# Kernel tuning notes

Hardware: AMD Instinct MI355X
Metric: run time of the kernel (lower is better)

## Reference

```python
import jax, jax.numpy as jnp
import numpy as np

N, E, C_IN, C_HID, C_OUT = 50000, 800000, 128, 64, 40


def _glorot(key, fan_in, fan_out):
    lim = np.sqrt(6.0 / (fan_in + fan_out)).astype(np.float32)
    return jax.random.uniform(key, (fan_in, fan_out), jnp.float32, -lim, lim)


def setup_inputs() -> dict:
    key = jax.random.key(0)
    kf, ks, ko, k1, k2 = jax.random.split(key, 5)
    features = jax.random.normal(kf, (N, C_IN), jnp.float32)
    src = jax.random.randint(ks, (E,), 0, N, jnp.int64 if jax.config.jax_enable_x64 else jnp.int32)
    # guarantee no self loops so add_remaining_self_loops == append full diagonal
    off = jax.random.randint(ko, (E,), 0, N - 1, src.dtype)
    dst = (src + 1 + off) % N
    return {
        "features": features,
        "src": src,
        "dst": dst,
        "W1": _glorot(k1, C_IN, C_HID),
        "b1": jnp.zeros((C_HID,), jnp.float32),
        "W2": _glorot(k2, C_HID, C_OUT),
        "b2": jnp.zeros((C_OUT,), jnp.float32),
    }


def reference(features, src, dst, W1, b1, W2, b2):
    n = features.shape[0]
    loop = jnp.arange(n, dtype=src.dtype)
    s = jnp.concatenate([src, loop])  # source nodes j (with self loops)
    d = jnp.concatenate([dst, loop])  # target nodes i
    ones = jnp.ones(s.shape[0], features.dtype)
    deg = jax.ops.segment_sum(ones, d, num_segments=n)  # in-degree incl. loop, >=1
    dinv = jax.lax.rsqrt(deg)
    norm = dinv[s] * dinv[d]  # D^{-1/2} A_hat D^{-1/2}, per edge

    def gcn_conv(x, W, b):
        h = x @ W  # [n, out]
        msgs = norm[:, None] * h[s]  # edge-wise gather + scale
        return jax.ops.segment_sum(msgs, d, num_segments=n) + b  # scatter-add

    x = jax.nn.relu(gcn_conv(features, W1, b1))
    # dropout: eval mode (training=False) -> identity
    x = gcn_conv(x, W2, b2)
    return jax.nn.log_softmax(x, axis=1)
```

## Files before the change

### kernel.cpp

```cpp
#include <hip/hip_runtime.h>
#include <math.h>

#define C_IN  128
#define C_HID 64
#define C_OUT 40
#define H1DW  32
#define H2DW  20

#define BKT_SH 7
#define BKT_N  (1 << BKT_SH)
#define CHUNK  1024
#define EPT    (CHUNK / 256)

__device__ __forceinline__ float bf2f(unsigned short u) {
    return __uint_as_float(((unsigned int)u) << 16);
}
__device__ __forceinline__ unsigned short f2bf(float f) {
    unsigned int x = __float_as_uint(f);
    return (unsigned short)((x + 0x7FFFu + ((x >> 16) & 1u)) >> 16);
}

__global__ void k_hist(const int* __restrict__ dst, int* __restrict__ hist2d, int e, int nbkt) {
    __shared__ int hist[512];
    for (int i = threadIdx.x; i < nbkt; i += 256) hist[i] = 0;
    __syncthreads();
    int base = blockIdx.x * CHUNK;
#pragma unroll
    for (int j = 0; j < EPT; ++j) {
        int i = base + j * 256 + threadIdx.x;
        if (i < e) atomicAdd(&hist[dst[i] >> BKT_SH], 1);
    }
    __syncthreads();
    int* row = hist2d + (size_t)blockIdx.x * nbkt;
    for (int i = threadIdx.x; i < nbkt; i += 256) row[i] = hist[i];
}

__global__ void k_bktscan(const int* __restrict__ hist2d, int* __restrict__ base2d,
                          int* __restrict__ tot, int nchunks, int nbkt) {
    __shared__ int wtot[4];
    const int b = blockIdx.x;
    const int t = threadIdx.x;
    const int lane = t & 63, wv = t >> 6;
    int carry = 0;
    for (int c0 = 0; c0 < nchunks; c0 += 256) {
        int c = c0 + t;
        int v = (c < nchunks) ? hist2d[(size_t)c * nbkt + b] : 0;
        int inc = v;
        for (int o = 1; o < 64; o <<= 1) { int u = __shfl_up(inc, o); if (lane >= o) inc += u; }
        if (lane == 63) wtot[wv] = inc;
        __syncthreads();
        int add = carry;
        for (int k = 0; k < wv; ++k) add += wtot[k];
        if (c < nchunks) base2d[(size_t)c * nbkt + b] = add + inc - v;
        carry += wtot[0] + wtot[1] + wtot[2] + wtot[3];
        __syncthreads();
    }
    if (t == 0) tot[b] = carry;
}

__global__ void k_scan_bkt(const int* __restrict__ tot, int* __restrict__ bstart, int nbkt, int e) {
    __shared__ int wtot[4];
    const int t = threadIdx.x;
    const int lane = t & 63, wv = t >> 6;
    int carry = 0;
    for (int b0 = 0; b0 < nbkt; b0 += 256) {
        int b = b0 + t;
        int v = (b < nbkt) ? tot[b] : 0;
        int inc = v;
        for (int o = 1; o < 64; o <<= 1) { int u = __shfl_up(inc, o); if (lane >= o) inc += u; }
        if (lane == 63) wtot[wv] = inc;
        __syncthreads();
        int add = carry;
        for (int k = 0; k < wv; ++k) add += wtot[k];
        if (b < nbkt) bstart[b] = add + inc - v;
        carry += wtot[0] + wtot[1] + wtot[2] + wtot[3];
        __syncthreads();
    }
    if (t == 0) bstart[nbkt] = e;
}

__global__ void k_binA(const int* __restrict__ src, const int* __restrict__ dst,
                       const int* __restrict__ bstart, const int* __restrict__ hist2d,
                       const int* __restrict__ base2d, unsigned int* __restrict__ bpack,
                       int e, int nbkt) {
    __shared__ int hist[512];
    __shared__ int excl[512];
    __shared__ int gbase[512];
    __shared__ int wtot[4];
    __shared__ unsigned int stage[CHUNK];
    const int t = threadIdx.x;
    const int base = blockIdx.x * CHUNK;
    const int lane = t & 63, wv = t >> 6;

    int carry = 0;
    for (int b0 = 0; b0 < nbkt; b0 += 256) {
        int b = b0 + t;
        int v = (b < nbkt) ? hist2d[(size_t)blockIdx.x * nbkt + b] : 0;
        int inc = v;
        for (int o = 1; o < 64; o <<= 1) { int u = __shfl_up(inc, o); if (lane >= o) inc += u; }
        if (lane == 63) wtot[wv] = inc;
        __syncthreads();
        int add = carry;
        for (int k = 0; k < wv; ++k) add += wtot[k];
        if (b < nbkt) {
            excl[b]  = add + inc - v;
            hist[b]  = 0;
            gbase[b] = bstart[b] + base2d[(size_t)blockIdx.x * nbkt + b];
        }
        carry += wtot[0] + wtot[1] + wtot[2] + wtot[3];
        __syncthreads();
    }

#pragma unroll
    for (int j = 0; j < EPT; ++j) {
        int i = base + j * 256 + t;
        if (i < e) {
            int d = dst[i];
            unsigned int pk = (unsigned int)src[i] | ((unsigned int)d << 16);
            int bk = d >> BKT_SH;
            int p  = excl[bk] + atomicAdd(&hist[bk], 1);
            stage[p] = pk;
        }
    }
    __syncthreads();

    int nchunk = min(CHUNK, e - base);
    for (int i = t; i < nchunk; i += 256) {
        unsigned int u = stage[i];
        int b = (int)(u >> 16) >> BKT_SH;
        bpack[gbase[b] + (i - excl[b])] = u;
    }
}

__global__ void k_binB(const int* __restrict__ bstart, const unsigned int* __restrict__ bpack,
                       int* __restrict__ row_start, float* __restrict__ dinv,
                       int* __restrict__ csr_src, int n, int e, int nbkt) {
    __shared__ int hist[BKT_N];
    __shared__ int excl[BKT_N];
    __shared__ int wtot[4];
    const int t = threadIdx.x;
    const int b = blockIdx.x;
    const int beg = bstart[b], end = bstart[b + 1];
    const int nodebase = b << BKT_SH;
    const int nloc = min(BKT_N, n - nodebase);

    for (int i = t; i < nloc; i += 256) hist[i] = 0;
    __syncthreads();
    for (int i = beg + t; i < end; i += 256)
        atomicAdd(&hist[(int)(bpack[i] >> 16) - nodebase], 1);
    __syncthreads();

    {
        int idx = t;
        int v = (idx < nloc) ? hist[idx] : 0;
        int inc = v; int lane = t & 63; int wv = t >> 6;
        for (int o = 1; o < 64; o <<= 1) { int u = __shfl_up(inc, o); if (lane >= o) inc += u; }
        if (lane == 63) wtot[wv] = inc;
        __syncthreads();
        int add = 0;
        for (int k = 0; k < wv; ++k) add += wtot[k];
        if (idx < nloc) excl[idx] = add + inc - v;
    }
    __syncthreads();

    for (int i = t; i < nloc; i += 256) {
        row_start[nodebase + i] = beg + excl[i];
        dinv[nodebase + i] = rsqrtf((float)hist[i] + 1.0f);
    }
    if (b == nbkt - 1 && t == 0) row_start[n] = e;
    __syncthreads();
    for (int i = t; i < nloc; i += 256) hist[i] = 0;
    __syncthreads();

    for (int i = beg + t; i < end; i += 256) {
        unsigned int u = bpack[i];
        int dl = (int)(u >> 16) - nodebase;
        int p = beg + excl[dl] + atomicAdd(&hist[dl], 1);
        csr_src[p] = (int)(u & 0xFFFFu);
    }
}

__global__ void k_gemm1(const float* __restrict__ X, const float* __restrict__ W1,
                        const float* __restrict__ dinv, unsigned short* __restrict__ h1b, int n) {
    __shared__ float xt[C_IN][64];
    __shared__ float wl[C_IN * C_HID];
    const int t = threadIdx.x;
    const int row0 = blockIdx.x * 64;

    for (int i = t; i < C_IN * C_HID; i += 256) wl[i] = W1[i];
    {
        int r = t >> 2, q = t & 3;
        int grow = row0 + r;
        for (int j = 0; j < 8; ++j) {
            int k = q * 32 + j * 4;
            float4 v = make_float4(0.f, 0.f, 0.f, 0.f);
            if (grow < n) v = *(const float4*)(X + (size_t)grow * C_IN + k);
            xt[k + 0][r] = v.x; xt[k + 1][r] = v.y; xt[k + 2][r] = v.z; xt[k + 3][r] = v.w;
        }
    }
    __syncthreads();

    const int rg = t >> 4, cg = t & 15;
    const int r0 = rg * 4, c0 = cg * 4;
    float acc[4][4] = {};
#pragma unroll 4
    for (int k = 0; k < C_IN; ++k) {
        float4 a = *(const float4*)&xt[k][r0];
        float4 b = *(const float4*)&wl[k * C_HID + c0];
        acc[0][0] = fmaf(a.x, b.x, acc[0][0]); acc[0][1] = fmaf(a.x, b.y, acc[0][1]);
        acc[0][2] = fmaf(a.x, b.z, acc[0][2]); acc[0][3] = fmaf(a.x, b.w, acc[0][3]);
        acc[1][0] = fmaf(a.y, b.x, acc[1][0]); acc[1][1] = fmaf(a.y, b.y, acc[1][1]);
        acc[1][2] = fmaf(a.y, b.z, acc[1][2]); acc[1][3] = fmaf(a.y, b.w, acc[1][3]);
        acc[2][0] = fmaf(a.z, b.x, acc[2][0]); acc[2][1] = fmaf(a.z, b.y, acc[2][1]);
        acc[2][2] = fmaf(a.z, b.z, acc[2][2]); acc[2][3] = fmaf(a.z, b.w, acc[2][3]);
        acc[3][0] = fmaf(a.w, b.x, acc[3][0]); acc[3][1] = fmaf(a.w, b.y, acc[3][1]);
        acc[3][2] = fmaf(a.w, b.z, acc[3][2]); acc[3][3] = fmaf(a.w, b.w, acc[3][3]);
    }
#pragma unroll
    for (int i = 0; i < 4; ++i) {
        int row = row0 + r0 + i;
        if (row < n) {
            float di = dinv[row];
            ushort4 o;
            o.x = f2bf(di * acc[i][0]); o.y = f2bf(di * acc[i][1]);
            o.z = f2bf(di * acc[i][2]); o.w = f2bf(di * acc[i][3]);
            *(ushort4*)(h1b + (size_t)row * C_HID + c0) = o;
        }
    }
}

__global__ void k_agg1(const int* __restrict__ row_start, const int* __restrict__ csr_src,
                       const unsigned short* __restrict__ h1b, const float* __restrict__ dinv,
                       const float* __restrict__ b1, unsigned int* __restrict__ out1d, int n) {
    const int t = threadIdx.x;
    const int wid  = t >> 6;
    const int lane = t & 63;
    const int node = blockIdx.x * 4 + wid;
    if (node >= n) return;

    const int h  = lane >> 5;
    const int c2 = lane & 31;
    const unsigned int* h1d = (const unsigned int*)h1b;

    int beg = row_start[node], end = row_start[node + 1];
    float alo[4] = {0.f, 0.f, 0.f, 0.f}, ahi[4] = {0.f, 0.f, 0.f, 0.f};
    {
        unsigned int u = h1d[(size_t)node * H1DW + c2];
        if (h == 0) {
            alo[0] = __uint_as_float(u << 16);
            ahi[0] = __uint_as_float(u & 0xFFFF0000u);
        }
    }
    for (int j = beg; j < end; j += 64) {
        int sv = (j + lane < end) ? csr_src[j + lane] : 0;
        int m  = min(64, end - j);
        for (int k = 0; k < m; k += 8) {
#pragma unroll
            for (int i = 0; i < 4; ++i) {
                int idx = k + 2 * i + h;
                int s   = __shfl(sv, idx);
                float f = (idx < m) ? 1.f : 0.f;
                unsigned int u = h1d[(size_t)s * H1DW + c2];
                alo[i] = fmaf(f, __uint_as_float(u << 16), alo[i]);
                ahi[i] = fmaf(f, __uint_as_float(u & 0xFFFF0000u), ahi[i]);
            }
        }
    }
    float lo = (alo[0] + alo[1]) + (alo[2] + alo[3]);
    float hi = (ahi[0] + ahi[1]) + (ahi[2] + ahi[3]);
    lo += __shfl_xor(lo, 32);
    hi += __shfl_xor(hi, 32);

    if (h == 0) {
        float di = dinv[node];
        float2 bb = *(const float2*)(b1 + 2 * c2);
        float vlo = di * lo + bb.x;
        float vhi = di * hi + bb.y;
        vlo = vlo > 0.f ? vlo : 0.f;
        vhi = vhi > 0.f ? vhi : 0.f;
        out1d[(size_t)node * H1DW + c2] =
            (unsigned int)f2bf(vlo) | ((unsigned int)f2bf(vhi) << 16);
    }
}

__global__ void k_gemm2(const unsigned int* __restrict__ out1d, const float* __restrict__ W2,
                        const float* __restrict__ dinv, unsigned int* __restrict__ h2d, int n) {
    __shared__ float xt[C_HID][96];
    __shared__ float wl[C_HID * C_OUT];
    const int t = threadIdx.x;
    const int row0 = blockIdx.x * 96;

    for (int i = t; i < C_HID * C_OUT; i += 256) wl[i] = W2[i];
    for (int idx = t; idx < 96 * H1DW; idx += 256) {
        int r = idx >> 5, d = idx & 31;
        int grow = row0 + r;
        unsigned int u = (grow < n) ? out1d[(size_t)grow * H1DW + d] : 0u;
        xt[2 * d][r]     = __uint_as_float(u << 16);
        xt[2 * d + 1][r] = __uint_as_float(u & 0xFFFF0000u);
    }
    __syncthreads();

    if (t >= 240) return;
    const int rg = t / 10, cg = t - rg * 10;
    const int r0 = rg * 4, c0 = cg * 4;
    float acc[4][4] = {};
#pragma unroll 4
    for (int k = 0; k < C_HID; ++k) {
        float4 a = *(const float4*)&xt[k][r0];
        float4 b = *(const float4*)&wl[k * C_OUT + c0];
        acc[0][0] = fmaf(a.x, b.x, acc[0][0]); acc[0][1] = fmaf(a.x, b.y, acc[0][1]);
        acc[0][2] = fmaf(a.x, b.z, acc[0][2]); acc[0][3] = fmaf(a.x, b.w, acc[0][3]);
        acc[1][0] = fmaf(a.y, b.x, acc[1][0]); acc[1][1] = fmaf(a.y, b.y, acc[1][1]);
        acc[1][2] = fmaf(a.y, b.z, acc[1][2]); acc[1][3] = fmaf(a.y, b.w, acc[1][3]);
        acc[2][0] = fmaf(a.z, b.x, acc[2][0]); acc[2][1] = fmaf(a.z, b.y, acc[2][1]);
        acc[2][2] = fmaf(a.z, b.z, acc[2][2]); acc[2][3] = fmaf(a.z, b.w, acc[2][3]);
        acc[3][0] = fmaf(a.w, b.x, acc[3][0]); acc[3][1] = fmaf(a.w, b.y, acc[3][1]);
        acc[3][2] = fmaf(a.w, b.z, acc[3][2]); acc[3][3] = fmaf(a.w, b.w, acc[3][3]);
    }
#pragma unroll
    for (int i = 0; i < 4; ++i) {
        int row = row0 + r0 + i;
        if (row < n) {
            float di = dinv[row];
            unsigned int u0 = (unsigned int)f2bf(di * acc[i][0]) | ((unsigned int)f2bf(di * acc[i][1]) << 16);
            unsigned int u1 = (unsigned int)f2bf(di * acc[i][2]) | ((unsigned int)f2bf(di * acc[i][3]) << 16);
            h2d[(size_t)row * H2DW + (c0 >> 1)]     = u0;
            h2d[(size_t)row * H2DW + (c0 >> 1) + 1] = u1;
        }
    }
}

__global__ void k_agg2(const int* __restrict__ row_start, const int* __restrict__ csr_src,
                       const unsigned short* __restrict__ h2b, const float* __restrict__ dinv,
                       const float* __restrict__ b2, float* __restrict__ out, int n) {
    int node = (blockIdx.x * 256 + threadIdx.x) >> 6;
    int lane = threadIdx.x & 63;
    if (node >= n) return;
    const int h3 = lane / 20;
    const int c2 = lane - h3 * 20;
    const unsigned int* h2d = (const unsigned int*)h2b;

    int beg = row_start[node], end = row_start[node + 1];
    float alo[4] = {0.f, 0.f, 0.f, 0.f}, ahi[4] = {0.f, 0.f, 0.f, 0.f};
    if (h3 == 0) {
        unsigned int u = h2d[(size_t)node * H2DW + c2];
        alo[0] = __uint_as_float(u << 16);
        ahi[0] = __uint_as_float(u & 0xFFFF0000u);
    }
    for (int j = beg; j < end; j += 64) {
        int sv = (j + lane < end) ? csr_src[j + lane] : 0;
        int m = min(64, end - j);
        for (int k = 0; k < m; k += 12) {
#pragma unroll
            for (int i = 0; i < 4; ++i) {
                int idx = k + 3 * i + h3;
                int s = __shfl(sv, idx & 63);
                float f = (idx < m) ? 1.f : 0.f;
                unsigned int u = h2d[(size_t)s * H2DW + c2];
                alo[i] = fmaf(f, __uint_as_float(u << 16), alo[i]);
                ahi[i] = fmaf(f, __uint_as_float(u & 0xFFFF0000u), ahi[i]);
            }
        }
    }
    float lo = (alo[0] + alo[1]) + (alo[2] + alo[3]);
    float hi = (ahi[0] + ahi[1]) + (ahi[2] + ahi[3]);
    float lA = __shfl(lo, c2 + 20), lB = __shfl(lo, c2 + 40);
    float hA = __shfl(hi, c2 + 20), hB = __shfl(hi, c2 + 40);
    lo += lA + lB;
    hi += hA + hB;

    float di = dinv[node];
    float vlo = -INFINITY, vhi = -INFINITY, ex = 0.f;
    if (h3 == 0) {
        float2 bb = *(const float2*)(b2 + 2 * c2);
        vlo = di * lo + bb.x;
        vhi = di * hi + bb.y;
    }
    float mx = fmaxf(vlo, vhi);
    for (int off = 16; off; off >>= 1) mx = fmaxf(mx, __shfl_xor(mx, off));
    if (h3 == 0) ex = expf(vlo - mx) + expf(vhi - mx);
    float ss = ex;
    for (int off = 16; off; off >>= 1) ss += __shfl_xor(ss, off);
    float lse = mx + logf(ss);
    if (h3 == 0)
        *(float2*)(out + (size_t)node * C_OUT + 2 * c2) = make_float2(vlo - lse, vhi - lse);
}

extern "C" void kernel_launch(void* const* d_in, const int* in_sizes, int n_in,
                              void* d_out, int out_size, void* d_ws, size_t ws_size,
                              hipStream_t stream) {
    const float* X   = (const float*)d_in[0];
    const int*   src = (const int*)d_in[1];
    const int*   dst = (const int*)d_in[2];
    const float* W1  = (const float*)d_in[3];
    const float* b1  = (const float*)d_in[4];
    const float* W2  = (const float*)d_in[5];
    const float* b2  = (const float*)d_in[6];
    float* out = (float*)d_out;

    const int N = in_sizes[0] / C_IN;
    const int E = in_sizes[1];
    const int NBKT = (N + BKT_N - 1) >> BKT_SH;
    const int nchunks = (E + CHUNK - 1) / CHUNK;

    char* ws = (char*)d_ws;
    size_t off = 0;
    auto take = [&](size_t bytes) { char* p = ws + off; off = (off + bytes + 255) & ~(size_t)255; return p; };
    int*   hist2d    = (int*)  take((size_t)nchunks * NBKT * 4);
    int*   base2d    = (int*)  take((size_t)nchunks * NBKT * 4);
    int*   tot       = (int*)  take(512 * 4);
    int*   bstart    = (int*)  take(512 * 4);
    unsigned int* bpack = (unsigned int*)take((size_t)E * 4);
    int*   csr_src   = (int*)  take((size_t)E * 4);
    int*   row_start = (int*)  take((size_t)(N + 1) * 4);
    float* dinv      = (float*)take((size_t)N * 4);
    unsigned short* h1b  = (unsigned short*)take((size_t)N * C_HID * 2);
    unsigned int*   out1 = (unsigned int*)  take((size_t)N * H1DW * 4);
    unsigned int*   h2d  = (unsigned int*)  take((size_t)N * H2DW * 4);

    k_hist    <<<nchunks, 256, 0, stream>>>(dst, hist2d, E, NBKT);
    k_bktscan <<<NBKT, 256, 0, stream>>>(hist2d, base2d, tot, nchunks, NBKT);
    k_scan_bkt<<<1, 256, 0, stream>>>(tot, bstart, NBKT, E);
    k_binA    <<<nchunks, 256, 0, stream>>>(src, dst, bstart, hist2d, base2d, bpack, E, NBKT);
    k_binB    <<<NBKT, 256, 0, stream>>>(bstart, bpack, row_start, dinv, csr_src, N, E, NBKT);

    k_gemm1   <<<(N + 63) / 64, 256, 0, stream>>>(X, W1, dinv, h1b, N);
    k_agg1    <<<(N + 3) / 4, 256, 0, stream>>>(row_start, csr_src, h1b, dinv, b1, out1, N);
    k_gemm2   <<<(N + 95) / 96, 256, 0, stream>>>(out1, W2, dinv, h2d, N);
    k_agg2    <<<((size_t)N * 64 + 255) / 256, 256, 0, stream>>>(row_start, csr_src,
                                                                 (const unsigned short*)h2d, dinv, b2, out, N);
}
```

Before: 123.9 us.

## Split feature tables into column halves and aggregate each half in separate passes

The bf16 feature tables for both layers are split into low and high column halves stored as separate arrays. Each aggregation runs as two passes, each gathering only half the columns. The intent is to shrink the randomly gathered working set so each half fits better in L2/MALL. The cost is reading the CSR twice, more kernel launches, and an extra float2 buffer passed between the two layer-2 passes before log_softmax.

```diff
diff --git a/kernel.cpp b/kernel.cpp
--- a/kernel.cpp
+++ b/kernel.cpp
@@ -4,17 +4,14 @@
 #define C_IN  128
 #define C_HID 64
 #define C_OUT 40
-#define H1DW  32
-#define H2DW  20
 
 #define BKT_SH 7
 #define BKT_N  (1 << BKT_SH)
 #define CHUNK  1024
 #define EPT    (CHUNK / 256)
 
-__device__ __forceinline__ float bf2f(unsigned short u) {
-    return __uint_as_float(((unsigned int)u) << 16);
-}
+__device__ __forceinline__ float bfLO(unsigned int u) { return __uint_as_float(u << 16); }
+__device__ __forceinline__ float bfHI(unsigned int u) { return __uint_as_float(u & 0xFFFF0000u); }
 __device__ __forceinline__ unsigned short f2bf(float f) {
     unsigned int x = __float_as_uint(f);
     return (unsigned short)((x + 0x7FFFu + ((x >> 16) & 1u)) >> 16);
@@ -181,7 +178,8 @@
 }
 
 __global__ void k_gemm1(const float* __restrict__ X, const float* __restrict__ W1,
-                        const float* __restrict__ dinv, unsigned short* __restrict__ h1b, int n) {
+                        const float* __restrict__ dinv,
+                        unsigned short* __restrict__ h1lo, unsigned short* __restrict__ h1hi, int n) {
     __shared__ float xt[C_IN][64];
     __shared__ float wl[C_IN * C_HID];
     const int t = threadIdx.x;
@@ -224,79 +222,72 @@
             ushort4 o;
             o.x = f2bf(di * acc[i][0]); o.y = f2bf(di * acc[i][1]);
             o.z = f2bf(di * acc[i][2]); o.w = f2bf(di * acc[i][3]);
-            *(ushort4*)(h1b + (size_t)row * C_HID + c0) = o;
-        }
-    }
-}
-
-__global__ void k_agg1(const int* __restrict__ row_start, const int* __restrict__ csr_src,
-                       const unsigned short* __restrict__ h1b, const float* __restrict__ dinv,
-                       const float* __restrict__ b1, unsigned int* __restrict__ out1d, int n) {
-    const int t = threadIdx.x;
-    const int wid  = t >> 6;
-    const int lane = t & 63;
+            if (c0 < 32) *(ushort4*)(h1lo + (size_t)row * 32 + c0)        = o;
+            else         *(ushort4*)(h1hi + (size_t)row * 32 + (c0 - 32)) = o;
+        }
+    }
+}
+
+template<int HALF>
+__global__ void k_agg1h(const int* __restrict__ row_start, const int* __restrict__ csr_src,
+                        const unsigned int* __restrict__ h1h, const float* __restrict__ dinv,
+                        const float* __restrict__ b1, unsigned int* __restrict__ out1h, int n) {
+    const int t = threadIdx.x;
+    const int wid = t >> 6, lane = t & 63;
     const int node = blockIdx.x * 4 + wid;
     if (node >= n) return;
-
-    const int h  = lane >> 5;
-    const int c2 = lane & 31;
-    const unsigned int* h1d = (const unsigned int*)h1b;
+    const int h4 = lane >> 4;
+    const int c2 = lane & 15;
 
     int beg = row_start[node], end = row_start[node + 1];
-    float alo[4] = {0.f, 0.f, 0.f, 0.f}, ahi[4] = {0.f, 0.f, 0.f, 0.f};
+    float alo0 = 0.f, ahi0 = 0.f, alo1 = 0.f, ahi1 = 0.f;
     {
-        unsigned int u = h1d[(size_t)node * H1DW + c2];
-        if (h == 0) {
-            alo[0] = __uint_as_float(u << 16);
-            ahi[0] = __uint_as_float(u & 0xFFFF0000u);
-        }
+        unsigned int u = h1h[(size_t)node * 16 + c2];
+        if (h4 == 0) { alo0 = bfLO(u); ahi0 = bfHI(u); }
     }
     for (int j = beg; j < end; j += 64) {
         int sv = (j + lane < end) ? csr_src[j + lane] : 0;
         int m  = min(64, end - j);
         for (int k = 0; k < m; k += 8) {
-#pragma unroll
-            for (int i = 0; i < 4; ++i) {
-                int idx = k + 2 * i + h;
-                int s   = __shfl(sv, idx);
-                float f = (idx < m) ? 1.f : 0.f;
-                unsigned int u = h1d[(size_t)s * H1DW + c2];
-                alo[i] = fmaf(f, __uint_as_float(u << 16), alo[i]);
-                ahi[i] = fmaf(f, __uint_as_float(u & 0xFFFF0000u), ahi[i]);
-            }
-        }
-    }
-    float lo = (alo[0] + alo[1]) + (alo[2] + alo[3]);
-    float hi = (ahi[0] + ahi[1]) + (ahi[2] + ahi[3]);
-    lo += __shfl_xor(lo, 32);
-    hi += __shfl_xor(hi, 32);
-
-    if (h == 0) {
+            int i0 = k + h4, i1 = k + 4 + h4;
+            int s0 = __shfl(sv, i0), s1 = __shfl(sv, i1);
+            float f0 = (i0 < m) ? 1.f : 0.f;
+            float f1 = (i1 < m) ? 1.f : 0.f;
+            unsigned int u0 = h1h[(size_t)s0 * 16 + c2];
+            unsigned int u1 = h1h[(size_t)s1 * 16 + c2];
+            alo0 = fmaf(f0, bfLO(u0), alo0); ahi0 = fmaf(f0, bfHI(u0), ahi0);
+            alo1 = fmaf(f1, bfLO(u1), alo1); ahi1 = fmaf(f1, bfHI(u1), ahi1);
+        }
+    }
+    float lo = alo0 + alo1, hi = ahi0 + ahi1;
+    lo += __shfl_xor(lo, 16); hi += __shfl_xor(hi, 16);
+    lo += __shfl_xor(lo, 32); hi += __shfl_xor(hi, 32);
+
+    if (h4 == 0) {
         float di = dinv[node];
-        float2 bb = *(const float2*)(b1 + 2 * c2);
-        float vlo = di * lo + bb.x;
-        float vhi = di * hi + bb.y;
-        vlo = vlo > 0.f ? vlo : 0.f;
-        vhi = vhi > 0.f ? vhi : 0.f;
-        out1d[(size_t)node * H1DW + c2] =
-            (unsigned int)f2bf(vlo) | ((unsigned int)f2bf(vhi) << 16);
-    }
-}
-
-__global__ void k_gemm2(const unsigned int* __restrict__ out1d, const float* __restrict__ W2,
-                        const float* __restrict__ dinv, unsigned int* __restrict__ h2d, int n) {
+        float2 bb = *(const float2*)(b1 + HALF * 32 + 2 * c2);
+        float vlo = fmaxf(fmaf(di, lo, bb.x), 0.f);
+        float vhi = fmaxf(fmaf(di, hi, bb.y), 0.f);
+        out1h[(size_t)node * 16 + c2] = (unsigned int)f2bf(vlo) | ((unsigned int)f2bf(vhi) << 16);
+    }
+}
+
+__global__ void k_gemm2(const unsigned int* __restrict__ o1lo, const unsigned int* __restrict__ o1hi,
+                        const float* __restrict__ W2, const float* __restrict__ dinv,
+                        unsigned int* __restrict__ h2lo, unsigned int* __restrict__ h2hi, int n) {
     __shared__ float xt[C_HID][96];
     __shared__ float wl[C_HID * C_OUT];
     const int t = threadIdx.x;
     const int row0 = blockIdx.x * 96;
 
     for (int i = t; i < C_HID * C_OUT; i += 256) wl[i] = W2[i];
-    for (int idx = t; idx < 96 * H1DW; idx += 256) {
-        int r = idx >> 5, d = idx & 31;
+    for (int idx = t; idx < 96 * 16; idx += 256) {
+        int r = idx >> 4, d = idx & 15;
         int grow = row0 + r;
-        unsigned int u = (grow < n) ? out1d[(size_t)grow * H1DW + d] : 0u;
-        xt[2 * d][r]     = __uint_as_float(u << 16);
-        xt[2 * d + 1][r] = __uint_as_float(u & 0xFFFF0000u);
+        unsigned int ulo = (grow < n) ? o1lo[(size_t)grow * 16 + d] : 0u;
+        unsigned int uhi = (grow < n) ? o1hi[(size_t)grow * 16 + d] : 0u;
+        xt[2 * d][r]      = bfLO(ulo); xt[2 * d + 1][r]  = bfHI(ulo);
+        xt[32 + 2 * d][r] = bfLO(uhi); xt[33 + 2 * d][r] = bfHI(uhi);
     }
     __syncthreads();
 
@@ -324,66 +315,84 @@
             float di = dinv[row];
             unsigned int u0 = (unsigned int)f2bf(di * acc[i][0]) | ((unsigned int)f2bf(di * acc[i][1]) << 16);
             unsigned int u1 = (unsigned int)f2bf(di * acc[i][2]) | ((unsigned int)f2bf(di * acc[i][3]) << 16);
-            h2d[(size_t)row * H2DW + (c0 >> 1)]     = u0;
-            h2d[(size_t)row * H2DW + (c0 >> 1) + 1] = u1;
-        }
-    }
-}
-
-__global__ void k_agg2(const int* __restrict__ row_start, const int* __restrict__ csr_src,
-                       const unsigned short* __restrict__ h2b, const float* __restrict__ dinv,
-                       const float* __restrict__ b2, float* __restrict__ out, int n) {
-    int node = (blockIdx.x * 256 + threadIdx.x) >> 6;
-    int lane = threadIdx.x & 63;
+            if (c0 < 20) {
+                h2lo[(size_t)row * 10 + (c0 >> 1)]     = u0;
+                h2lo[(size_t)row * 10 + (c0 >> 1) + 1] = u1;
+            } else {
+                h2hi[(size_t)row * 10 + ((c0 - 20) >> 1)]     = u0;
+                h2hi[(size_t)row * 10 + ((c0 - 20) >> 1) + 1] = u1;
+            }
+        }
+    }
+}
+
+template<int PASS>
+__global__ void k_agg2h(const int* __restrict__ row_start, const int* __restrict__ csr_src,
+                        const unsigned int* __restrict__ h2h, const float* __restrict__ dinv,
+                        const float* __restrict__ b2, float2* __restrict__ accLo,
+                        float* __restrict__ out, int n) {
+    const int t = threadIdx.x;
+    const int wid = t >> 6, lane = t & 63;
+    const int node = blockIdx.x * 4 + wid;
     if (node >= n) return;
-    const int h3 = lane / 20;
-    const int c2 = lane - h3 * 20;
-    const unsigned int* h2d = (const unsigned int*)h2b;
+    const int h6 = lane / 10;
+    const int c2 = lane - h6 * 10;
+    const bool act = h6 < 6;
 
     int beg = row_start[node], end = row_start[node + 1];
-    float alo[4] = {0.f, 0.f, 0.f, 0.f}, ahi[4] = {0.f, 0.f, 0.f, 0.f};
-    if (h3 == 0) {
-        unsigned int u = h2d[(size_t)node * H2DW + c2];
-        alo[0] = __uint_as_float(u << 16);
-        ahi[0] = __uint_as_float(u & 0xFFFF0000u);
+    float alo0 = 0.f, ahi0 = 0.f, alo1 = 0.f, ahi1 = 0.f;
+    if (h6 == 0) {
+        unsigned int u = h2h[(size_t)node * 10 + c2];
+        alo0 = bfLO(u); ahi0 = bfHI(u);
     }
     for (int j = beg; j < end; j += 64) {
         int sv = (j + lane < end) ? csr_src[j + lane] : 0;
-        int m = min(64, end - j);
+        int m  = min(64, end - j);
         for (int k = 0; k < m; k += 12) {
-#pragma unroll
-            for (int i = 0; i < 4; ++i) {
-                int idx = k + 3 * i + h3;
-                int s = __shfl(sv, idx & 63);
-                float f = (idx < m) ? 1.f : 0.f;
-                unsigned int u = h2d[(size_t)s * H2DW + c2];
-                alo[i] = fmaf(f, __uint_as_float(u << 16), alo[i]);
-                ahi[i] = fmaf(f, __uint_as_float(u & 0xFFFF0000u), ahi[i]);
-            }
-        }
-    }
-    float lo = (alo[0] + alo[1]) + (alo[2] + alo[3]);
-    float hi = (ahi[0] + ahi[1]) + (ahi[2] + ahi[3]);
-    float lA = __shfl(lo, c2 + 20), lB = __shfl(lo, c2 + 40);
-    float hA = __shfl(hi, c2 + 20), hB = __shfl(hi, c2 + 40);
-    lo += lA + lB;
-    hi += hA + hB;
-
-    float di = dinv[node];
-    float vlo = -INFINITY, vhi = -INFINITY, ex = 0.f;
-    if (h3 == 0) {
-        float2 bb = *(const float2*)(b2 + 2 * c2);
-        vlo = di * lo + bb.x;
-        vhi = di * hi + bb.y;
-    }
-    float mx = fmaxf(vlo, vhi);
-    for (int off = 16; off; off >>= 1) mx = fmaxf(mx, __shfl_xor(mx, off));
-    if (h3 == 0) ex = expf(vlo - mx) + expf(vhi - mx);
-    float ss = ex;
-    for (int off = 16; off; off >>= 1) ss += __shfl_xor(ss, off);
-    float lse = mx + logf(ss);
-    if (h3 == 0)
-        *(float2*)(out + (size_t)node * C_OUT + 2 * c2) = make_float2(vlo - lse, vhi - lse);
+            int i0 = k + h6, i1 = k + 6 + h6;
+            int s0 = __shfl(sv, i0 & 63), s1 = __shfl(sv, i1 & 63);
+            float f0 = (act && i0 < m) ? 1.f : 0.f;
+            float f1 = (act && i1 < m) ? 1.f : 0.f;
+            unsigned int u0 = h2h[(size_t)s0 * 10 + c2];
+            unsigned int u1 = h2h[(size_t)s1 * 10 + c2];
+            alo0 = fmaf(f0, bfLO(u0), alo0); ahi0 = fmaf(f0, bfHI(u0), ahi0);
+            alo1 = fmaf(f1, bfLO(u1), alo1); ahi1 = fmaf(f1, bfHI(u1), ahi1);
+        }
+    }
+    float plo = alo0 + alo1, phi = ahi0 + ahi1;
+    float lo = 0.f, hi = 0.f;
+#pragma unroll
+    for (int g = 0; g < 6; ++g) {
+        lo += __shfl(plo, c2 + 10 * g);
+        hi += __shfl(phi, c2 + 10 * g);
+    }
+
+    if (PASS == 0) {
+        if (lane < 10) accLo[(size_t)node * 10 + c2] = make_float2(lo, hi);
+    } else {
+        float di = dinv[node];
+        float vA = -INFINITY, vB = -INFINITY, vC = -INFINITY, vD = -INFINITY;
+        if (lane < 10) {
+            float2 p = accLo[(size_t)node * 10 + c2];
+            vA = fmaf(di, p.x, b2[2 * c2]);
+            vB = fmaf(di, p.y, b2[2 * c2 + 1]);
+            vC = fmaf(di, lo,  b2[20 + 2 * c2]);
+            vD = fmaf(di, hi,  b2[21 + 2 * c2]);
+        }
+        float mx = fmaxf(fmaxf(vA, vB), fmaxf(vC, vD));
+#pragma unroll
+        for (int off = 1; off <= 8; off <<= 1) mx = fmaxf(mx, __shfl_xor(mx, off));
+        float es = 0.f;
+        if (lane < 10)
+            es = expf(vA - mx) + expf(vB - mx) + expf(vC - mx) + expf(vD - mx);
+#pragma unroll
+        for (int off = 1; off <= 8; off <<= 1) es += __shfl_xor(es, off);
+        float lse = mx + logf(es);
+        if (lane < 10) {
+            *(float2*)(out + (size_t)node * C_OUT + 2 * c2)      = make_float2(vA - lse, vB - lse);
+            *(float2*)(out + (size_t)node * C_OUT + 20 + 2 * c2) = make_float2(vC - lse, vD - lse);
+        }
+    }
 }
 
 extern "C" void kernel_launch(void* const* d_in, const int* in_sizes, int n_in,
@@ -414,9 +423,13 @@
     int*   csr_src   = (int*)  take((size_t)E * 4);
     int*   row_start = (int*)  take((size_t)(N + 1) * 4);
     float* dinv      = (float*)take((size_t)N * 4);
-    unsigned short* h1b  = (unsigned short*)take((size_t)N * C_HID * 2);
-    unsigned int*   out1 = (unsigned int*)  take((size_t)N * H1DW * 4);
-    unsigned int*   h2d  = (unsigned int*)  take((size_t)N * H2DW * 4);
+    unsigned short* h1lo  = (unsigned short*)take((size_t)N * 32 * 2);
+    unsigned short* h1hi  = (unsigned short*)take((size_t)N * 32 * 2);
+    unsigned int*   out1lo = (unsigned int*)take((size_t)N * 16 * 4);
+    unsigned int*   out1hi = (unsigned int*)take((size_t)N * 16 * 4);
+    unsigned int*   h2lo   = (unsigned int*)take((size_t)N * 10 * 4);
+    unsigned int*   h2hi   = (unsigned int*)take((size_t)N * 10 * 4);
+    float2*         accLo  = (float2*)      take((size_t)N * 10 * 8);
 
     k_hist    <<<nchunks, 256, 0, stream>>>(dst, hist2d, E, NBKT);
     k_bktscan <<<NBKT, 256, 0, stream>>>(hist2d, base2d, tot, nchunks, NBKT);
@@ -424,9 +437,12 @@
     k_binA    <<<nchunks, 256, 0, stream>>>(src, dst, bstart, hist2d, base2d, bpack, E, NBKT);
     k_binB    <<<NBKT, 256, 0, stream>>>(bstart, bpack, row_start, dinv, csr_src, N, E, NBKT);
 
-    k_gemm1   <<<(N + 63) / 64, 256, 0, stream>>>(X, W1, dinv, h1b, N);
-    k_agg1    <<<(N + 3) / 4, 256, 0, stream>>>(row_start, csr_src, h1b, dinv, b1, out1, N);
-    k_gemm2   <<<(N + 95) / 96, 256, 0, stream>>>(out1, W2, dinv, h2d, N);
-    k_agg2    <<<((size_t)N * 64 + 255) / 256, 256, 0, stream>>>(row_start, csr_src,
-                                                                 (const unsigned short*)h2d, dinv, b2, out, N);
-}
+    k_gemm1   <<<(N + 63) / 64, 256, 0, stream>>>(X, W1, dinv, h1lo, h1hi, N);
+    k_agg1h<0><<<(N + 3) / 4, 256, 0, stream>>>(row_start, csr_src, (const unsigned int*)h1lo,
+                                                dinv, b1, out1lo, N);
+    k_agg1h<1><<<(N + 3) / 4, 256, 0, stream>>>(row_start, csr_src, (const unsigned int*)h1hi,
+                                                dinv, b1, out1hi, N);
+    k_gemm2   <<<(N + 95) / 96, 256, 0, stream>>>(out1lo, out1hi, W2, dinv, h2lo, h2hi, N);
+    k_agg2h<0><<<(N + 3) / 4, 256, 0, stream>>>(row_start, csr_src, h2lo, dinv, b2, accLo, out, N);
+    k_agg2h<1><<<(N + 3) / 4, 256, 0, stream>>>(row_start, csr_src, h2hi, dinv, b2, accLo, out, N);
+}
```

After: 153.7 us. +24.1%, slower.
